# Performance work log

Hardware: AMD Instinct MI355X
Metric: run time of the kernel (lower is better)

Reference implementation:

```python
import jax, jax.numpy as jnp
import numpy as np

BITS = 4
MAXQ = (1 << BITS) - 1          # 15
PACK = 32 // BITS               # 8 values per int32
GROUP = 128
CLIPMIN = 1e-5
CLIPMAX = 1e4


def _unpack_rows(qweight, infeatures):
    # qweight: [in/PACK, out] int32; values packed along the row (infeatures) dim.
    shifts = (jnp.arange(PACK, dtype=jnp.int32) * BITS)[None, :, None]   # [1,PACK,1]
    w = (qweight[:, None, :] >> shifts) & MAXQ                            # [in/PACK, PACK, out]
    return w.reshape(-1, qweight.shape[1])[:infeatures].astype(jnp.float32)


def setup_inputs() -> dict:
    key = jax.random.key(0)
    k1, k2, k3, k4, k5 = jax.random.split(key, 5)
    infeatures, outfeatures, tokens = 4096, 4096, 2048
    num_groups = infeatures // GROUP
    x = jax.random.normal(k1, (tokens, infeatures), dtype=jnp.float32)
    # positive scales, well inside [CLIPMIN, CLIPMAX]
    scales = jax.random.uniform(k2, (num_groups, outfeatures), dtype=jnp.float32,
                                minval=0.005, maxval=0.02)
    # zero points roughly centered in the quant range [0, 15]
    zero_points = jax.random.uniform(k3, (num_groups, outfeatures), dtype=jnp.float32,
                                     minval=0.0, maxval=float(MAXQ))
    bias = jax.random.normal(k4, (outfeatures,), dtype=jnp.float32)
    qweight = jax.random.randint(k5, (infeatures // PACK, outfeatures),
                                 jnp.iinfo(jnp.int32).min, jnp.iinfo(jnp.int32).max,
                                 dtype=jnp.int32)
    return {"x": x, "scales": scales, "zero_points": zero_points,
            "bias": bias, "qweight": qweight}


def reference(x, scales, zero_points, bias, qweight):
    infeatures = x.shape[-1]
    out_f = scales.shape[1]
    num_groups = scales.shape[0]
    w = _unpack_rows(qweight, infeatures)                       # [in, out] fp32 in [0,15]
    s = jnp.clip(scales, CLIPMIN, CLIPMAX)                      # [G, out]
    z = jnp.clip(jnp.round(zero_points), 0.0, float(MAXQ))      # [G, out]
    wg = w.reshape(num_groups, GROUP, out_f)                    # [G, group, out]
    deq = ((wg - z[:, None, :]) * s[:, None, :]).reshape(infeatures, out_f)
    return x @ deq + bias
```

## Files before the change

kernel.cpp:

```cpp
#include <hip/hip_runtime.h>
#include <cstdint>
#include <cstddef>

typedef __attribute__((ext_vector_type(8))) short short8;
typedef __attribute__((ext_vector_type(4))) float floatx4;

typedef __attribute__((address_space(1))) const void gvoid_t;
typedef __attribute__((address_space(3))) void lvoid_t;

__device__ inline short f2bf(float f) {
    unsigned u = __float_as_uint(f);
    u = (u + 0x7FFFu + ((u >> 16) & 1u)) >> 16;
    return (short)u;
}

__global__ __launch_bounds__(256) void convert_x_kernel(
    const float* __restrict__ x, short* __restrict__ xb, long long n)
{
    long long i = ((long long)blockIdx.x * 256 + threadIdx.x) * 8;
    if (i + 8 > n) return;
    const float4* p = (const float4*)(x + i);
    float4 v0 = p[0];
    float4 v1 = p[1];
    short8 h;
    h[0] = f2bf(v0.x); h[1] = f2bf(v0.y); h[2] = f2bf(v0.z); h[3] = f2bf(v0.w);
    h[4] = f2bf(v1.x); h[5] = f2bf(v1.y); h[6] = f2bf(v1.z); h[7] = f2bf(v1.w);
    *(short8*)(xb + i) = h;
}

__global__ __launch_bounds__(256) void dequant_kernel(
    const int* __restrict__ qw, const float* __restrict__ scales,
    const float* __restrict__ zps, short* __restrict__ deqT,
    int N, int K)
{
    __shared__ int lds_q[32 * 65];
    const int t  = threadIdx.x;
    const int n0 = blockIdx.x * 64;
    const int r0 = blockIdx.y * 32;

    #pragma unroll
    for (int v = 0; v < 2; ++v) {
        int idx = t + v * 256;
        int row = idx >> 4;
        int c4  = (idx & 15) * 4;
        const int4 q4 = *(const int4*)(qw + (size_t)(r0 + row) * N + n0 + c4);
        int base = row * 65 + c4;
        lds_q[base + 0] = q4.x;
        lds_q[base + 1] = q4.y;
        lds_q[base + 2] = q4.z;
        lds_q[base + 3] = q4.w;
    }
    __syncthreads();

    const int nl = t >> 2;
    const int rc = (t & 3) * 8;
    const int g  = (r0 >> 4) + ((t & 3) >> 1);

    float s = scales[(size_t)g * N + n0 + nl];
    s = fminf(fmaxf(s, 1e-5f), 1e4f);
    float z = rintf(zps[(size_t)g * N + n0 + nl]);
    z = fminf(fmaxf(z, 0.0f), 15.0f);

    short* outp = deqT + (size_t)(n0 + nl) * K + (size_t)(r0 + rc) * 8;
    #pragma unroll
    for (int i = 0; i < 8; ++i) {
        int q = lds_q[(rc + i) * 65 + nl];
        short8 h;
        #pragma unroll
        for (int j = 0; j < 8; ++j) {
            float f = (float)((q >> (4 * j)) & 15);
            h[j] = f2bf((f - z) * s);
        }
        *(short8*)(outp + i * 8) = h;
    }
}

#define BM 128
#define BN 128
#define BK 64

__global__ __launch_bounds__(256) void gemm_bf16_bt(
    const short* __restrict__ A, const short* __restrict__ Bt,
    const float* __restrict__ bias, float* __restrict__ C,
    int M, int N, int K)
{
    __shared__ __align__(16) short a_lds[BM * BK];
    __shared__ __align__(16) short b_lds[BN * BK];

    const int t  = threadIdx.x;
    const int L  = t & 63;
    const int w  = t >> 6;
    const int m0 = blockIdx.y * BM;
    const int n0 = blockIdx.x * BN;
    const int wm = (w & 1) * 64;
    const int wn = (w >> 1) * 64;

    floatx4 acc[4][4] = {};

    const int sr = L >> 3;
    const int sc = L & 7;
    const int gc = sc ^ sr;
    const short* ag = A  + (size_t)(m0 + w * 8 + sr) * K + gc * 8;
    const short* bg = Bt + (size_t)(n0 + w * 8 + sr) * K + gc * 8;
    short* a_dst = a_lds + (w * 8) * BK;
    short* b_dst = b_lds + (w * 8) * BK;

    for (int kt = 0; kt < K; kt += BK) {
        #pragma unroll
        for (int i = 0; i < 4; ++i) {
            __builtin_amdgcn_global_load_lds(
                (gvoid_t*)(ag + (size_t)i * 32 * K + kt),
                (lvoid_t*)(a_dst + i * 32 * BK), 16, 0, 0);
            __builtin_amdgcn_global_load_lds(
                (gvoid_t*)(bg + (size_t)i * 32 * K + kt),
                (lvoid_t*)(b_dst + i * 32 * BK), 16, 0, 0);
        }
        __syncthreads();

        #pragma unroll
        for (int s = 0; s < 2; ++s) {
            const int p = ((s * 4) + (L >> 4)) ^ (L & 7);
            short8 af[4], bfr[4];
            #pragma unroll
            for (int i = 0; i < 4; ++i)
                af[i] = *(const short8*)(a_lds + (wm + 16 * i + (L & 15)) * BK + p * 8);
            #pragma unroll
            for (int j = 0; j < 4; ++j)
                bfr[j] = *(const short8*)(b_lds + (wn + 16 * j + (L & 15)) * BK + p * 8);
            #pragma unroll
            for (int i = 0; i < 4; ++i) {
                #pragma unroll
                for (int j = 0; j < 4; ++j)
                    acc[i][j] = __builtin_amdgcn_mfma_f32_16x16x32_bf16(
                        af[i], bfr[j], acc[i][j], 0, 0, 0);
            }
        }
        __syncthreads();
    }

    float bv[4];
    #pragma unroll
    for (int j = 0; j < 4; ++j)
        bv[j] = bias[n0 + wn + 16 * j + (L & 15)];
    const int col0 = n0 + wn + (L & 15);
    #pragma unroll
    for (int i = 0; i < 4; ++i) {
        const int row0 = m0 + wm + 16 * i + (L >> 4) * 4;
        #pragma unroll
        for (int r = 0; r < 4; ++r) {
            float* outr = C + (size_t)(row0 + r) * N + col0;
            #pragma unroll
            for (int j = 0; j < 4; ++j)
                outr[16 * j] = acc[i][j][r] + bv[j];
        }
    }
}

extern "C" void kernel_launch(void* const* d_in, const int* in_sizes, int n_in,
                              void* d_out, int out_size, void* d_ws, size_t ws_size,
                              hipStream_t stream)
{
    const float* x      = (const float*)d_in[0];
    const float* scales = (const float*)d_in[1];
    const float* zps    = (const float*)d_in[2];
    const float* bias   = (const float*)d_in[3];
    const int*   qw     = (const int*)d_in[4];

    const int N = in_sizes[3];
    const int G = in_sizes[1] / N;
    const int K = G * 128;
    const int M = in_sizes[0] / K;

    short* xb   = (short*)d_ws;
    short* deqT = xb + (size_t)M * K;
    float* out  = (float*)d_out;

    const long long nx = (long long)M * K;
    convert_x_kernel<<<(int)(nx / 2048), 256, 0, stream>>>(x, xb, nx);
    dequant_kernel<<<dim3(N / 64, K / 256), 256, 0, stream>>>(qw, scales, zps, deqT, N, K);
    gemm_bf16_bt<<<dim3(N / BN, M / BM), 256, 0, stream>>>(xb, deqT, bias, out, M, N, K);
}
```

Baseline: 190.4 us.

## Fuse int4 dequantization into fp16 GEMM with double-buffered activation tiles

```diff
diff --git a/kernel.cpp b/kernel.cpp
--- a/kernel.cpp
+++ b/kernel.cpp
@@ -2,90 +2,57 @@
 #include <cstdint>
 #include <cstddef>
 
-typedef __attribute__((ext_vector_type(8))) short short8;
+typedef __attribute__((ext_vector_type(2))) _Float16 half2v;
+typedef __attribute__((ext_vector_type(8))) _Float16 half8;
 typedef __attribute__((ext_vector_type(4))) float floatx4;
 
 typedef __attribute__((address_space(1))) const void gvoid_t;
 typedef __attribute__((address_space(3))) void lvoid_t;
 
-__device__ inline short f2bf(float f) {
-    unsigned u = __float_as_uint(f);
-    u = (u + 0x7FFFu + ((u >> 16) & 1u)) >> 16;
-    return (short)u;
-}
-
 __global__ __launch_bounds__(256) void convert_x_kernel(
-    const float* __restrict__ x, short* __restrict__ xb, long long n)
+    const float* __restrict__ x, _Float16* __restrict__ xh, long long n)
 {
     long long i = ((long long)blockIdx.x * 256 + threadIdx.x) * 8;
     if (i + 8 > n) return;
     const float4* p = (const float4*)(x + i);
-    float4 v0 = p[0];
-    float4 v1 = p[1];
-    short8 h;
-    h[0] = f2bf(v0.x); h[1] = f2bf(v0.y); h[2] = f2bf(v0.z); h[3] = f2bf(v0.w);
-    h[4] = f2bf(v1.x); h[5] = f2bf(v1.y); h[6] = f2bf(v1.z); h[7] = f2bf(v1.w);
-    *(short8*)(xb + i) = h;
-}
-
-__global__ __launch_bounds__(256) void dequant_kernel(
-    const int* __restrict__ qw, const float* __restrict__ scales,
-    const float* __restrict__ zps, short* __restrict__ deqT,
-    int N, int K)
-{
-    __shared__ int lds_q[32 * 65];
-    const int t  = threadIdx.x;
-    const int n0 = blockIdx.x * 64;
-    const int r0 = blockIdx.y * 32;
-
-    #pragma unroll
-    for (int v = 0; v < 2; ++v) {
-        int idx = t + v * 256;
-        int row = idx >> 4;
-        int c4  = (idx & 15) * 4;
-        const int4 q4 = *(const int4*)(qw + (size_t)(r0 + row) * N + n0 + c4);
-        int base = row * 65 + c4;
-        lds_q[base + 0] = q4.x;
-        lds_q[base + 1] = q4.y;
-        lds_q[base + 2] = q4.z;
-        lds_q[base + 3] = q4.w;
-    }
-    __syncthreads();
-
-    const int nl = t >> 2;
-    const int rc = (t & 3) * 8;
-    const int g  = (r0 >> 4) + ((t & 3) >> 1);
-
-    float s = scales[(size_t)g * N + n0 + nl];
-    s = fminf(fmaxf(s, 1e-5f), 1e4f);
-    float z = rintf(zps[(size_t)g * N + n0 + nl]);
-    z = fminf(fmaxf(z, 0.0f), 15.0f);
-
-    short* outp = deqT + (size_t)(n0 + nl) * K + (size_t)(r0 + rc) * 8;
-    #pragma unroll
-    for (int i = 0; i < 8; ++i) {
-        int q = lds_q[(rc + i) * 65 + nl];
-        short8 h;
-        #pragma unroll
-        for (int j = 0; j < 8; ++j) {
-            float f = (float)((q >> (4 * j)) & 15);
-            h[j] = f2bf((f - z) * s);
-        }
-        *(short8*)(outp + i * 8) = h;
-    }
+    float4 a = p[0];
+    float4 b = p[1];
+    half8 h;
+    h[0] = (_Float16)a.x; h[1] = (_Float16)b.x;
+    h[2] = (_Float16)a.y; h[3] = (_Float16)b.y;
+    h[4] = (_Float16)a.z; h[5] = (_Float16)b.z;
+    h[6] = (_Float16)a.w; h[7] = (_Float16)b.w;
+    *(half8*)(xh + i) = h;
 }
 
 #define BM 128
 #define BN 128
 #define BK 64
 
-__global__ __launch_bounds__(256) void gemm_bf16_bt(
-    const short* __restrict__ A, const short* __restrict__ Bt,
+__device__ inline half8 unpack8(int q, half2v sh, half2v ch)
+{
+    unsigned uq = (unsigned)q;
+    unsigned p0 = (uq & 0x000F000Fu) | 0x64006400u;
+    unsigned p1 = ((uq >> 4) & 0x000F000Fu) | 0x64006400u;
+    unsigned p2 = ((uq >> 8) & 0x000F000Fu) | 0x64006400u;
+    unsigned p3 = ((uq >> 12) & 0x000F000Fu) | 0x64006400u;
+    half2v v0 = (__builtin_bit_cast(half2v, p0) - ch) * sh;
+    half2v v1 = (__builtin_bit_cast(half2v, p1) - ch) * sh;
+    half2v v2 = (__builtin_bit_cast(half2v, p2) - ch) * sh;
+    half2v v3 = (__builtin_bit_cast(half2v, p3) - ch) * sh;
+    half8 r;
+    r[0] = v0[0]; r[1] = v0[1]; r[2] = v1[0]; r[3] = v1[1];
+    r[4] = v2[0]; r[5] = v2[1]; r[6] = v3[0]; r[7] = v3[1];
+    return r;
+}
+
+__global__ __launch_bounds__(256) void gemm_fused(
+    const _Float16* __restrict__ A, const int* __restrict__ qw,
+    const float* __restrict__ scales, const float* __restrict__ zps,
     const float* __restrict__ bias, float* __restrict__ C,
     int M, int N, int K)
 {
-    __shared__ __align__(16) short a_lds[BM * BK];
-    __shared__ __align__(16) short b_lds[BN * BK];
+    __shared__ __align__(16) _Float16 a_lds[2][BM * BK];
 
     const int t  = threadIdx.x;
     const int L  = t & 63;
@@ -100,49 +67,121 @@
     const int sr = L >> 3;
     const int sc = L & 7;
     const int gc = sc ^ sr;
-    const short* ag = A  + (size_t)(m0 + w * 8 + sr) * K + gc * 8;
-    const short* bg = Bt + (size_t)(n0 + w * 8 + sr) * K + gc * 8;
-    short* a_dst = a_lds + (w * 8) * BK;
-    short* b_dst = b_lds + (w * 8) * BK;
-
-    for (int kt = 0; kt < K; kt += BK) {
-        #pragma unroll
-        for (int i = 0; i < 4; ++i) {
+    const _Float16* ag = A + (size_t)(m0 + w * 8 + sr) * K + gc * 8;
+    const int dst = (w * 8) * BK;
+
+    const int nc = n0 + wn + (L & 15);
+    const int* qp = qw + (size_t)(L >> 4) * N + nc;
+    const float* sp = scales + nc;
+    const float* zp = zps + nc;
+
+    const int NG = K / 128;
+
+    #pragma unroll
+    for (int i = 0; i < 4; ++i)
+        __builtin_amdgcn_global_load_lds(
+            (gvoid_t*)(ag + (size_t)i * 32 * K),
+            (lvoid_t*)(&a_lds[0][dst + i * 32 * BK]), 16, 0, 0);
+
+    int qc[8], qm[8];
+    #pragma unroll
+    for (int s2 = 0; s2 < 2; ++s2)
+        #pragma unroll
+        for (int j = 0; j < 4; ++j)
+            qc[s2 * 4 + j] = qp[(size_t)(s2 * 4) * N + 16 * j];
+
+    half2v sh[4], ch[4];
+    {
+        #pragma unroll
+        for (int j = 0; j < 4; ++j) {
+            float s = fminf(fmaxf(sp[16 * j], 1e-5f), 1e4f);
+            float z = fminf(fmaxf(rintf(zp[16 * j]), 0.0f), 15.0f);
+            _Float16 hs = (_Float16)s;
+            _Float16 hc = (_Float16)(1024.0f + z);
+            sh[j][0] = hs; sh[j][1] = hs;
+            ch[j][0] = hc; ch[j][1] = hc;
+        }
+    }
+
+    auto compute = [&](int cur, const int* qarr) {
+        #pragma unroll
+        for (int s2 = 0; s2 < 2; ++s2) {
+            const int p = (s2 * 4 + (L >> 4)) ^ (L & 7);
+            half8 af[4];
+            #pragma unroll
+            for (int i = 0; i < 4; ++i)
+                af[i] = *(const half8*)(&a_lds[cur][(wm + 16 * i + (L & 15)) * BK + p * 8]);
+            #pragma unroll
+            for (int j = 0; j < 4; ++j) {
+                half8 bf = unpack8(qarr[s2 * 4 + j], sh[j], ch[j]);
+                #pragma unroll
+                for (int i = 0; i < 4; ++i)
+                    acc[i][j] = __builtin_amdgcn_mfma_f32_16x16x32_f16(
+                        af[i], bf, acc[i][j], 0, 0, 0);
+            }
+        }
+    };
+
+    for (int g = 0; g < NG; ++g) {
+        const int t1 = 2 * g + 1;
+
+        __syncthreads();
+
+        #pragma unroll
+        for (int i = 0; i < 4; ++i)
             __builtin_amdgcn_global_load_lds(
-                (gvoid_t*)(ag + (size_t)i * 32 * K + kt),
-                (lvoid_t*)(a_dst + i * 32 * BK), 16, 0, 0);
-            __builtin_amdgcn_global_load_lds(
-                (gvoid_t*)(bg + (size_t)i * 32 * K + kt),
-                (lvoid_t*)(b_dst + i * 32 * BK), 16, 0, 0);
-        }
+                (gvoid_t*)(ag + (size_t)i * 32 * K + (size_t)t1 * BK),
+                (lvoid_t*)(&a_lds[1][dst + i * 32 * BK]), 16, 0, 0);
+        #pragma unroll
+        for (int s2 = 0; s2 < 2; ++s2)
+            #pragma unroll
+            for (int j = 0; j < 4; ++j)
+                qm[s2 * 4 + j] = qp[(size_t)(t1 * 8 + s2 * 4) * N + 16 * j];
+
+        compute(0, qc);
+
         __syncthreads();
 
-        #pragma unroll
-        for (int s = 0; s < 2; ++s) {
-            const int p = ((s * 4) + (L >> 4)) ^ (L & 7);
-            short8 af[4], bfr[4];
+        float snf[4], znf[4];
+        if (g + 1 < NG) {
+            const int t2 = 2 * g + 2;
             #pragma unroll
             for (int i = 0; i < 4; ++i)
-                af[i] = *(const short8*)(a_lds + (wm + 16 * i + (L & 15)) * BK + p * 8);
-            #pragma unroll
-            for (int j = 0; j < 4; ++j)
-                bfr[j] = *(const short8*)(b_lds + (wn + 16 * j + (L & 15)) * BK + p * 8);
-            #pragma unroll
-            for (int i = 0; i < 4; ++i) {
+                __builtin_amdgcn_global_load_lds(
+                    (gvoid_t*)(ag + (size_t)i * 32 * K + (size_t)t2 * BK),
+                    (lvoid_t*)(&a_lds[0][dst + i * 32 * BK]), 16, 0, 0);
+            #pragma unroll
+            for (int s2 = 0; s2 < 2; ++s2)
                 #pragma unroll
                 for (int j = 0; j < 4; ++j)
-                    acc[i][j] = __builtin_amdgcn_mfma_f32_16x16x32_bf16(
-                        af[i], bfr[j], acc[i][j], 0, 0, 0);
+                    qc[s2 * 4 + j] = qp[(size_t)(t2 * 8 + s2 * 4) * N + 16 * j];
+            #pragma unroll
+            for (int j = 0; j < 4; ++j) {
+                snf[j] = sp[(size_t)(g + 1) * N + 16 * j];
+                znf[j] = zp[(size_t)(g + 1) * N + 16 * j];
             }
         }
-        __syncthreads();
+
+        compute(1, qm);
+
+        if (g + 1 < NG) {
+            #pragma unroll
+            for (int j = 0; j < 4; ++j) {
+                float s = fminf(fmaxf(snf[j], 1e-5f), 1e4f);
+                float z = fminf(fmaxf(rintf(znf[j]), 0.0f), 15.0f);
+                _Float16 hs = (_Float16)s;
+                _Float16 hc = (_Float16)(1024.0f + z);
+                sh[j][0] = hs; sh[j][1] = hs;
+                ch[j][0] = hc; ch[j][1] = hc;
+            }
+        }
     }
 
     float bv[4];
     #pragma unroll
     for (int j = 0; j < 4; ++j)
-        bv[j] = bias[n0 + wn + 16 * j + (L & 15)];
-    const int col0 = n0 + wn + (L & 15);
+        bv[j] = bias[nc + 16 * j];
+    const int col0 = nc;
     #pragma unroll
     for (int i = 0; i < 4; ++i) {
         const int row0 = m0 + wm + 16 * i + (L >> 4) * 4;
@@ -171,12 +210,11 @@
     const int K = G * 128;
     const int M = in_sizes[0] / K;
 
-    short* xb   = (short*)d_ws;
-    short* deqT = xb + (size_t)M * K;
-    float* out  = (float*)d_out;
+    _Float16* xh = (_Float16*)d_ws;
+    float* out   = (float*)d_out;
 
     const long long nx = (long long)M * K;
-    convert_x_kernel<<<(int)(nx / 2048), 256, 0, stream>>>(x, xb, nx);
-    dequant_kernel<<<dim3(N / 64, K / 256), 256, 0, stream>>>(qw, scales, zps, deqT, N, K);
-    gemm_bf16_bt<<<dim3(N / BN, M / BM), 256, 0, stream>>>(xb, deqT, bias, out, M, N, K);
-}
+    convert_x_kernel<<<(int)(nx / 2048), 256, 0, stream>>>(x, xh, nx);
+    gemm_fused<<<dim3(N / BN, M / BM), 256, 0, stream>>>(
+        xh, qw, scales, zps, bias, out, M, N, K);
+}
```

New measurement: 193.4 us. No clear change (+1.6%).
